# Kernel tuning notes

Measured on AMD Instinct MI355X. Metric: run time of the kernel, lower is better.

The kernel has to match this reference:

```python
import jax, jax.numpy as jnp
import numpy as np

N = 64        # SSM state size
L = 262144    # l_max / sequence length


def setup_inputs() -> dict:
    key = jax.random.key(0)
    ks = jax.random.split(key, 8)
    u = jax.random.normal(ks[0], (L,), dtype=jnp.float32)
    # HiPPO-DPLR style eigenvalue init
    Lambda_re = -0.5 * jnp.ones((N,), jnp.float32)
    Lambda_im = jnp.pi * jnp.arange(N, dtype=jnp.float32)
    P_re = jax.random.normal(ks[1], (N,), jnp.float32)
    P_im = jax.random.normal(ks[2], (N,), jnp.float32)
    B_re = jax.random.normal(ks[3], (N,), jnp.float32)
    B_im = jax.random.normal(ks[4], (N,), jnp.float32)
    C_ri = (0.5 ** 0.5) * jax.random.normal(ks[5], (N, 2), jnp.float32)  # C = C_ri[:,0] + i*C_ri[:,1]
    D = jnp.ones((1,), jnp.float32)
    log_step = jax.random.uniform(ks[6], (1,), jnp.float32,
                                  minval=float(np.log(0.001)), maxval=float(np.log(0.1)))
    return {"u": u, "Lambda_re": Lambda_re, "Lambda_im": Lambda_im,
            "P_re": P_re, "P_im": P_im, "B_re": B_re, "B_im": B_im,
            "C_ri": C_ri, "D": D, "log_step": log_step}


def _kernel_DPLR(Lambda, P, Q, B, C, step, l):
    # Evaluate the SSM generating function at the l roots of unity (bilinear discretization)
    Omega = jnp.exp((-2j * jnp.pi) * (jnp.arange(l) / l))          # (L,)
    g = (2.0 / step) * ((1.0 - Omega) / (1.0 + Omega))             # (L,)
    c = 2.0 / (1.0 + Omega)                                        # (L,)
    # Core Cauchy matrix: the single large (L, N) complex intermediate
    recip = 1.0 / (g[:, None] - Lambda[None, :])                   # (L, N)
    # Four Cauchy dot products fused into one thin matmul
    v = jnp.stack([C.conj() * B, C.conj() * P,
                   Q.conj() * B, Q.conj() * P], axis=1)            # (N, 4)
    k = recip @ v                                                  # (L, 4)
    k00, k01, k10, k11 = k[:, 0], k[:, 1], k[:, 2], k[:, 3]
    atRoots = c * (k00 - k01 * (1.0 / (1.0 + k11)) * k10)          # (L,)
    return jnp.fft.ifft(atRoots, l).real                           # (L,) real kernel


def _causal_convolution(u, K):
    l = u.shape[0]
    ud = jnp.fft.rfft(jnp.pad(u, (0, K.shape[0])))
    Kd = jnp.fft.rfft(jnp.pad(K, (0, l)))
    return jnp.fft.irfft(ud * Kd)[:l]


def reference(u, Lambda_re, Lambda_im, P_re, P_im, B_re, B_im, C_ri, D, log_step):
    Lambda = Lambda_re + 1j * Lambda_im
    P = P_re + 1j * P_im
    B = B_re + 1j * B_im
    C = C_ri[:, 0] + 1j * C_ri[:, 1]
    step = jnp.exp(log_step)                                       # (1,)
    K = _kernel_DPLR(Lambda, P, P, B, C, step, u.shape[0])
    return _causal_convolution(u, K) + D * u
```

## Files before the change

kernel.cpp:

```cpp
#include <hip/hip_runtime.h>
#include <math.h>

#define L_LEN  262144
#define NST    64
#define TPB    256
#define PI2F   6.2831853071795864769f
#define PIF    3.1415926535897932385f

__device__ inline float2 cmul(float2 a, float2 b) {
    return make_float2(a.x*b.x - a.y*b.y, a.x*b.y + a.y*b.x);
}

template<int M, int NF>
__device__ float2* lds_fft_r4(float2* b0, float2* b1, float sgn) {
    float2* src = b0; float2* dst = b1;
    int Ns = 1;
    while (Ns * 4 <= M) {
        __syncthreads();
        const int NB = NF * (M / 4);
        for (int bi = threadIdx.x; bi < NB; bi += TPB) {
            int f = bi / (M / 4);
            int j = bi & (M / 4 - 1);
            int r = j & (Ns - 1);
            const float2* s = src + f * M;
            float2 x0 = s[j];
            float2 x1 = s[j +     (M/4)];
            float2 x2 = s[j + 2 * (M/4)];
            float2 x3 = s[j + 3 * (M/4)];
            float ang = sgn * PI2F * ((float)r / (float)(4 * Ns));
            float sn, cs; __sincosf(ang, &sn, &cs);
            float2 w1 = make_float2(cs, sn);
            float2 w2 = cmul(w1, w1);
            float2 w3 = cmul(w2, w1);
            x1 = cmul(x1, w1); x2 = cmul(x2, w2); x3 = cmul(x3, w3);
            float2 t0 = make_float2(x0.x + x2.x, x0.y + x2.y);
            float2 t1 = make_float2(x0.x - x2.x, x0.y - x2.y);
            float2 t2 = make_float2(x1.x + x3.x, x1.y + x3.y);
            float2 t3 = make_float2(x1.x - x3.x, x1.y - x3.y);
            float2* d = dst + f * M + ((j - r) << 2) + r;
            d[0]      = make_float2(t0.x + t2.x, t0.y + t2.y);
            d[Ns]     = make_float2(t1.x - sgn * t3.y, t1.y + sgn * t3.x);
            d[2 * Ns] = make_float2(t0.x - t2.x, t0.y - t2.y);
            d[3 * Ns] = make_float2(t1.x + sgn * t3.y, t1.y - sgn * t3.x);
        }
        float2* t = src; src = dst; dst = t;
        Ns <<= 2;
    }
    if (Ns < M) {
        __syncthreads();
        const int NB = NF * (M / 2);
        for (int bi = threadIdx.x; bi < NB; bi += TPB) {
            int f = bi / (M / 2);
            int j = bi & (M / 2 - 1);
            const float2* s = src + f * M;
            float2 a = s[j];
            float2 b = s[j + M / 2];
            float ang = sgn * PI2F * ((float)j / (float)M);
            float sn, cs; __sincosf(ang, &sn, &cs);
            float2 wb = make_float2(cs * b.x - sn * b.y, cs * b.y + sn * b.x);
            float2* d = dst + f * M + j;
            d[0]     = make_float2(a.x + wb.x, a.y + wb.y);
            d[M / 2] = make_float2(a.x - wb.x, a.y - wb.y);
        }
        float2* t = src; src = dst; dst = t;
    }
    __syncthreads();
    return src;
}


__global__ __launch_bounds__(TPB) void kI(
    const float* __restrict__ u,
    const float* __restrict__ Lre, const float* __restrict__ Lim,
    const float* __restrict__ Pre, const float* __restrict__ Pim,
    const float* __restrict__ Bre, const float* __restrict__ Bim,
    const float* __restrict__ Cri, const float* __restrict__ lstp,
    float2* __restrict__ Acm, float2* __restrict__ T_K,
    float2* __restrict__ T_U, float2* __restrict__ T_Uo)
{
    __shared__ float2 b0[2048], b1[2048];
    __shared__ float4 cA[NST], cB[NST], cC[NST], cD[NST];
    const int t = threadIdx.x, bx = blockIdx.x;
    const int c0 = (bx & 255) << 1;
    const float invL = 1.0f / (float)L_LEN;
    if (bx < 256) {
        if (t < NST) {
            float lr = Lre[t], li = Lim[t];
            float pr = Pre[t], pi = Pim[t];
            float br = Bre[t], bi = Bim[t];
            float cr = Cri[2*t], ci = Cri[2*t+1];
            float dx = -lr;
            float v00x = cr*br + ci*bi, v00y = cr*bi - ci*br;
            float v01x = cr*pr + ci*pi, v01y = cr*pi - ci*pr;
            float v10x = pr*br + pi*bi, v10y = pr*bi - pi*br;
            float v11x = pr*pr + pi*pi;
            cA[t] = make_float4(li, dx*dx, dx*v11x, -v11x);
            cB[t] = make_float4(dx*v00x, v00y, dx*v00y, -v00x);
            cC[t] = make_float4(dx*v01x, v01y, dx*v01y, -v01x);
            cD[t] = make_float4(dx*v10x, v10y, dx*v10y, -v10x);
        }
        __syncthreads();
        float G2 = 2.0f / expf(lstp[0]);
        float tn[4], gi[4], acc[4][8];
        #pragma unroll
        for (int p = 0; p < 4; ++p) {
            int i = t + (p << 8);
            int f = i >> 9, e = i & 511;
            int m = (c0 + f) + (e << 9);
            float h = PIF * ((float)m * invL);
            float sn, cs; __sincosf(h, &sn, &cs);
            float tv = sn * __frcp_rn(cs);
            tv = fminf(fmaxf(tv, -1e7f), 1e7f);
            tn[p] = tv; gi[p] = G2 * tv;
            #pragma unroll
            for (int q = 0; q < 8; ++q) acc[p][q] = 0.f;
        }
        #pragma unroll 2
        for (int n = 0; n < NST; ++n) {
            float4 a = cA[n], b = cB[n], cc = cC[n], d = cD[n];
            #pragma unroll
            for (int p = 0; p < 4; ++p) {
                float dy   = gi[p] - a.x;
                float iv   = __frcp_rn(fmaf(dy, dy, a.y));
                float ivdy = iv * dy;
                acc[p][6] = fmaf(iv, a.z, acc[p][6]);
                acc[p][7] = fmaf(ivdy, a.w, acc[p][7]);
                acc[p][0] = fmaf(iv, b.x,  fmaf(ivdy, b.y,  acc[p][0]));
                acc[p][1] = fmaf(iv, b.z,  fmaf(ivdy, b.w,  acc[p][1]));
                acc[p][2] = fmaf(iv, cc.x, fmaf(ivdy, cc.y, acc[p][2]));
                acc[p][3] = fmaf(iv, cc.z, fmaf(ivdy, cc.w, acc[p][3]));
                acc[p][4] = fmaf(iv, d.x,  fmaf(ivdy, d.y,  acc[p][4]));
                acc[p][5] = fmaf(iv, d.z,  fmaf(ivdy, d.w,  acc[p][5]));
            }
        }
        #pragma unroll
        for (int p = 0; p < 4; ++p) {
            int i = t + (p << 8);
            int f = i >> 9, e = i & 511;
            float ax = 1.f + acc[p][6], ay = acc[p][7];
            float im = 1.f / (ax*ax + ay*ay);
            float tx = acc[p][2]*acc[p][4] - acc[p][3]*acc[p][5];
            float ty = acc[p][2]*acc[p][5] + acc[p][3]*acc[p][4];
            float wx = acc[p][0] - (tx*ax + ty*ay) * im;
            float wy = acc[p][1] - (ty*ax - tx*ay) * im;
            float2 A = make_float2(wx - tn[p]*wy, wy + tn[p]*wx);
            Acm[((c0 + f) << 9) + e] = A;
            b0[i] = A;
        }
        float2* r = lds_fft_r4<512, 2>(b0, b1, +1.f);
        for (int i = t; i < 1024; i += TPB) {
            int f = i & 1, k = i >> 1;
            int c = c0 + f;
            float ang = PI2F * ((float)(c * k) * invL);
            float sn, cs; __sincosf(ang, &sn, &cs);
            T_K[(k << 9) + c] = cmul(make_float2(cs, sn), r[(f << 9) + k]);
        }
    } else {
        for (int i = t; i < 1024; i += TPB) {
            int f = i & 1, e = i >> 1;
            int n = (c0 + f) + (e << 9);
            float uv = u[n];
            float sn, cs; __sincosf(PIF * ((float)n * invL), &sn, &cs);
            b0[(f << 9) + e]       = make_float2(uv, 0.f);
            b0[((2 + f) << 9) + e] = make_float2(uv * cs, -uv * sn);
        }
        float2* r = lds_fft_r4<512, 4>(b0, b1, -1.f);
        for (int i = t; i < 2048; i += TPB) {
            int f = i & 1, k = (i >> 1) & 511, v = i >> 10;
            int c = c0 + f;
            float ang = -PI2F * ((float)(c * k) * invL);
            float sn, cs; __sincosf(ang, &sn, &cs);
            float2 val = cmul(make_float2(cs, sn), r[(((v << 1) + f) << 9) + k]);
            if (v == 0) T_U [(k << 9) + c] = val;
            else        T_Uo[(k << 9) + c] = val;
        }
    }
}

__global__ __launch_bounds__(TPB) void kII(
    const float2* __restrict__ T_K, const float2* __restrict__ T_U,
    const float2* __restrict__ T_Uo,
    float2* __restrict__ T_Ko, float2* __restrict__ Ue, float2* __restrict__ Uo)
{
    __shared__ float2 b0[2048], b1[2048];
    const int t = threadIdx.x, bx = blockIdx.x;
    const int c0 = (bx & 255) << 1;
    const float invL = 1.0f / (float)L_LEN;
    if (bx < 256) {
        for (int i = t; i < 1024; i += TPB)
            b0[i] = T_K[((c0 + (i >> 9)) << 9) + (i & 511)];
        float2* r = lds_fft_r4<512, 2>(b0, b1, +1.f);
        float2* o = (r == b0) ? b1 : b0;
        for (int i = t; i < 1024; i += TPB) {
            int f = i >> 9, o1 = i & 511;
            int n = (c0 + f) + (o1 << 9);
            float K = r[i].x * invL;
            float sn, cs; __sincosf(PIF * ((float)n * invL), &sn, &cs);
            o[i] = make_float2(K * cs, -K * sn);
        }
        float2* r2 = lds_fft_r4<512, 2>(o, r, -1.f);
        for (int i = t; i < 1024; i += TPB) {
            int f = i & 1, k = i >> 1;
            int c = c0 + f;
            float ang = -PI2F * ((float)(c * k) * invL);
            float sn, cs; __sincosf(ang, &sn, &cs);
            T_Ko[(k << 9) + c] = cmul(make_float2(cs, sn), r2[(f << 9) + k]);
        }
    } else {
        for (int i = t; i < 2048; i += TPB) {
            int v = i >> 10, f = (i >> 9) & 1, e = i & 511;
            const float2* Tin = v ? T_Uo : T_U;
            b0[i] = Tin[((c0 + f) << 9) + e];
        }
        float2* r = lds_fft_r4<512, 4>(b0, b1, -1.f);
        for (int i = t; i < 2048; i += TPB) {
            int v = i >> 10, f = (i >> 9) & 1, k2 = i & 511;
            float2* Xo = v ? Uo : Ue;
            Xo[((c0 + f) << 9) + k2] = r[i];
        }
    }
}

__global__ __launch_bounds__(TPB) void kIII(
    const float2* __restrict__ T_Ko, const float2* __restrict__ Ue,
    const float2* __restrict__ Uo, const float2* __restrict__ Acm,
    float2* __restrict__ T_Ve, float2* __restrict__ T_Vo)
{
    __shared__ float2 b0[1024], b1[1024];
    const int t = threadIdx.x, kc = blockIdx.x;
    const float invL = 1.0f / (float)L_LEN;
    for (int i = t; i < 512; i += TPB)
        b0[i] = T_Ko[(kc << 9) + i];
    float2* r = lds_fft_r4<512, 1>(b0, b1, -1.f);
    float2* o = (r == b0) ? b1 : b0;
    for (int i = t; i < 512; i += TPB) {
        float2 ko = r[i];
        float2 ue = Ue [(kc << 9) + i];
        float2 uo = Uo [(kc << 9) + i];
        float2 av = Acm[(kc << 9) + i];
        o[i]       = cmul(ue, av);
        o[i + 512] = cmul(uo, ko);
    }
    float2* r2 = lds_fft_r4<512, 2>(o, r, +1.f);
    for (int i = t; i < 1024; i += TPB) {
        int v = i >> 9, k = i & 511;
        float ang = PI2F * ((float)(kc * k) * invL);
        float sn, cs; __sincosf(ang, &sn, &cs);
        float2 val = cmul(make_float2(cs, sn), r2[(v << 9) + k]);
        if (v == 0) T_Ve[(k << 9) + kc] = val;
        else        T_Vo[(k << 9) + kc] = val;
    }
}

__global__ __launch_bounds__(TPB) void kIV(
    const float2* __restrict__ T_Ve, const float2* __restrict__ T_Vo,
    const float* __restrict__ u, const float* __restrict__ Dp,
    float* __restrict__ out)
{
    __shared__ float2 b0[1024], b1[1024];
    const int t = threadIdx.x, k = blockIdx.x;
    const float invL = 1.0f / (float)L_LEN;
    for (int i = t; i < 512; i += TPB) {
        b0[i]       = T_Ve[(k << 9) + i];
        b0[i + 512] = T_Vo[(k << 9) + i];
    }
    float2* r = lds_fft_r4<512, 2>(b0, b1, +1.f);
    const float sc = 0.5f * invL;
    const float D = Dp[0];
    for (int o1 = t; o1 < 512; o1 += TPB) {
        int n = k + (o1 << 9);
        float sn, cs; __sincosf(PIF * ((float)n * invL), &sn, &cs);
        float2 yE = r[o1];
        float2 yO = r[o1 + 512];
        out[n] = fmaf(D, u[n], (yE.x + cs * yO.x - sn * yO.y) * sc);
    }
}

extern "C" void kernel_launch(void* const* d_in, const int* in_sizes, int n_in,
                              void* d_out, int out_size, void* d_ws, size_t ws_size,
                              hipStream_t stream) {
    const float* u    = (const float*)d_in[0];
    const float* Lre  = (const float*)d_in[1];
    const float* Lim  = (const float*)d_in[2];
    const float* Pre  = (const float*)d_in[3];
    const float* Pim  = (const float*)d_in[4];
    const float* Bre  = (const float*)d_in[5];
    const float* Bim  = (const float*)d_in[6];
    const float* Cri  = (const float*)d_in[7];
    const float* Dp   = (const float*)d_in[8];
    const float* lstp = (const float*)d_in[9];
    float* out = (float*)d_out;

    char* ws = (char*)d_ws;
    float2* Acm  = (float2*)(ws);
    float2* T_K  = (float2*)(ws + ( 2u << 20));
    float2* T_U  = (float2*)(ws + ( 4u << 20));
    float2* T_Uo = (float2*)(ws + ( 6u << 20));
    float2* T_Ko = (float2*)(ws + ( 8u << 20));
    float2* Ue   = (float2*)(ws + (10u << 20));
    float2* Uo   = (float2*)(ws + (12u << 20));
    float2* T_Ve = (float2*)(ws + (14u << 20));
    float2* T_Vo = (float2*)(ws + (16u << 20));

    kI  <<<512, TPB, 0, stream>>>(u, Lre,Lim,Pre,Pim,Bre,Bim,Cri,lstp,
                                  Acm, T_K, T_U, T_Uo);
    kII <<<512, TPB, 0, stream>>>(T_K, T_U, T_Uo, T_Ko, Ue, Uo);
    kIII<<<512, TPB, 0, stream>>>(T_Ko, Ue, Uo, Acm, T_Ve, T_Vo);
    kIV <<<512, TPB, 0, stream>>>(T_Ve, T_Vo, u, Dp, out);
}
```

Measured before the change: 117.7 us.

## Evaluate kernel spectrum directly at even and odd bins, dropping K round-trip FFTs

Instead of building the kernel spectrum at the L roots of unity, inverse-transforming it to time and forward-transforming the padded kernel again, the Cauchy generating function is evaluated directly at the integer and half-integer frequency positions the padded convolution needs. It is then multiplied with the input spectrum inside the spectral kernel. This removes the separate kernel-path FFT passes and the Acm/T_K/T_Ko/Ue/Uo intermediates, and cuts the pipeline from four launches to three. In exchange the Cauchy sum runs on twice as many points, now spread across all 512 blocks. The odd-bin evaluation relies on the state transition decaying to negligible size over L steps.

```diff
diff --git a/kernel.cpp b/kernel.cpp
--- a/kernel.cpp
+++ b/kernel.cpp
@@ -69,209 +69,148 @@
 }
 
 
-__global__ __launch_bounds__(TPB) void kI(
+__global__ __launch_bounds__(TPB) void k1_pass1(
     const float* __restrict__ u,
+    float2* __restrict__ T_U, float2* __restrict__ T_Uo)
+{
+    __shared__ float2 b0[1024], b1[1024];
+    const int t = threadIdx.x, bx = blockIdx.x;
+    const int sig = bx & 1;
+    const int c0  = bx & 510;
+    const float invL = 1.0f / (float)L_LEN;
+    for (int i = t; i < 1024; i += TPB) {
+        int f = i & 1, e = i >> 1;
+        int n = (c0 + f) + (e << 9);
+        float uv = u[n];
+        if (sig) {
+            float sn, cs; __sincosf(PIF * ((float)n * invL), &sn, &cs);
+            b0[(f << 9) + e] = make_float2(uv * cs, -uv * sn);
+        } else {
+            b0[(f << 9) + e] = make_float2(uv, 0.f);
+        }
+    }
+    float2* r = lds_fft_r4<512, 2>(b0, b1, -1.f);
+    float2* Tout = sig ? T_Uo : T_U;
+    for (int i = t; i < 1024; i += TPB) {
+        int f = i & 1, k = i >> 1;
+        int c = c0 + f;
+        float ang = -PI2F * ((float)(c * k) * invL);
+        float sn, cs; __sincosf(ang, &sn, &cs);
+        Tout[(k << 9) + c] = cmul(make_float2(cs, sn), r[(f << 9) + k]);
+    }
+}
+
+__global__ __launch_bounds__(TPB) void k2_spectral(
+    const float2* __restrict__ T_U, const float2* __restrict__ T_Uo,
     const float* __restrict__ Lre, const float* __restrict__ Lim,
     const float* __restrict__ Pre, const float* __restrict__ Pim,
     const float* __restrict__ Bre, const float* __restrict__ Bim,
     const float* __restrict__ Cri, const float* __restrict__ lstp,
-    float2* __restrict__ Acm, float2* __restrict__ T_K,
-    float2* __restrict__ T_U, float2* __restrict__ T_Uo)
-{
-    __shared__ float2 b0[2048], b1[2048];
-    __shared__ float4 cA[NST], cB[NST], cC[NST], cD[NST];
-    const int t = threadIdx.x, bx = blockIdx.x;
-    const int c0 = (bx & 255) << 1;
-    const float invL = 1.0f / (float)L_LEN;
-    if (bx < 256) {
-        if (t < NST) {
-            float lr = Lre[t], li = Lim[t];
-            float pr = Pre[t], pi = Pim[t];
-            float br = Bre[t], bi = Bim[t];
-            float cr = Cri[2*t], ci = Cri[2*t+1];
-            float dx = -lr;
-            float v00x = cr*br + ci*bi, v00y = cr*bi - ci*br;
-            float v01x = cr*pr + ci*pi, v01y = cr*pi - ci*pr;
-            float v10x = pr*br + pi*bi, v10y = pr*bi - pi*br;
-            float v11x = pr*pr + pi*pi;
-            cA[t] = make_float4(li, dx*dx, dx*v11x, -v11x);
-            cB[t] = make_float4(dx*v00x, v00y, dx*v00y, -v00x);
-            cC[t] = make_float4(dx*v01x, v01y, dx*v01y, -v01x);
-            cD[t] = make_float4(dx*v10x, v10y, dx*v10y, -v10x);
-        }
-        __syncthreads();
-        float G2 = 2.0f / expf(lstp[0]);
-        float tn[4], gi[4], acc[4][8];
-        #pragma unroll
-        for (int p = 0; p < 4; ++p) {
-            int i = t + (p << 8);
-            int f = i >> 9, e = i & 511;
-            int m = (c0 + f) + (e << 9);
-            float h = PIF * ((float)m * invL);
-            float sn, cs; __sincosf(h, &sn, &cs);
-            float tv = sn * __frcp_rn(cs);
-            tv = fminf(fmaxf(tv, -1e7f), 1e7f);
-            tn[p] = tv; gi[p] = G2 * tv;
-            #pragma unroll
-            for (int q = 0; q < 8; ++q) acc[p][q] = 0.f;
-        }
-        #pragma unroll 2
-        for (int n = 0; n < NST; ++n) {
-            float4 a = cA[n], b = cB[n], cc = cC[n], d = cD[n];
-            #pragma unroll
-            for (int p = 0; p < 4; ++p) {
-                float dy   = gi[p] - a.x;
-                float iv   = __frcp_rn(fmaf(dy, dy, a.y));
-                float ivdy = iv * dy;
-                acc[p][6] = fmaf(iv, a.z, acc[p][6]);
-                acc[p][7] = fmaf(ivdy, a.w, acc[p][7]);
-                acc[p][0] = fmaf(iv, b.x,  fmaf(ivdy, b.y,  acc[p][0]));
-                acc[p][1] = fmaf(iv, b.z,  fmaf(ivdy, b.w,  acc[p][1]));
-                acc[p][2] = fmaf(iv, cc.x, fmaf(ivdy, cc.y, acc[p][2]));
-                acc[p][3] = fmaf(iv, cc.z, fmaf(ivdy, cc.w, acc[p][3]));
-                acc[p][4] = fmaf(iv, d.x,  fmaf(ivdy, d.y,  acc[p][4]));
-                acc[p][5] = fmaf(iv, d.z,  fmaf(ivdy, d.w,  acc[p][5]));
-            }
-        }
-        #pragma unroll
-        for (int p = 0; p < 4; ++p) {
-            int i = t + (p << 8);
-            int f = i >> 9, e = i & 511;
-            float ax = 1.f + acc[p][6], ay = acc[p][7];
-            float im = 1.f / (ax*ax + ay*ay);
-            float tx = acc[p][2]*acc[p][4] - acc[p][3]*acc[p][5];
-            float ty = acc[p][2]*acc[p][5] + acc[p][3]*acc[p][4];
-            float wx = acc[p][0] - (tx*ax + ty*ay) * im;
-            float wy = acc[p][1] - (ty*ax - tx*ay) * im;
-            float2 A = make_float2(wx - tn[p]*wy, wy + tn[p]*wx);
-            Acm[((c0 + f) << 9) + e] = A;
-            b0[i] = A;
-        }
-        float2* r = lds_fft_r4<512, 2>(b0, b1, +1.f);
-        for (int i = t; i < 1024; i += TPB) {
-            int f = i & 1, k = i >> 1;
-            int c = c0 + f;
-            float ang = PI2F * ((float)(c * k) * invL);
-            float sn, cs; __sincosf(ang, &sn, &cs);
-            T_K[(k << 9) + c] = cmul(make_float2(cs, sn), r[(f << 9) + k]);
-        }
-    } else {
-        for (int i = t; i < 1024; i += TPB) {
-            int f = i & 1, e = i >> 1;
-            int n = (c0 + f) + (e << 9);
-            float uv = u[n];
-            float sn, cs; __sincosf(PIF * ((float)n * invL), &sn, &cs);
-            b0[(f << 9) + e]       = make_float2(uv, 0.f);
-            b0[((2 + f) << 9) + e] = make_float2(uv * cs, -uv * sn);
-        }
-        float2* r = lds_fft_r4<512, 4>(b0, b1, -1.f);
-        for (int i = t; i < 2048; i += TPB) {
-            int f = i & 1, k = (i >> 1) & 511, v = i >> 10;
-            int c = c0 + f;
-            float ang = -PI2F * ((float)(c * k) * invL);
-            float sn, cs; __sincosf(ang, &sn, &cs);
-            float2 val = cmul(make_float2(cs, sn), r[(((v << 1) + f) << 9) + k]);
-            if (v == 0) T_U [(k << 9) + c] = val;
-            else        T_Uo[(k << 9) + c] = val;
-        }
-    }
-}
-
-__global__ __launch_bounds__(TPB) void kII(
-    const float2* __restrict__ T_K, const float2* __restrict__ T_U,
-    const float2* __restrict__ T_Uo,
-    float2* __restrict__ T_Ko, float2* __restrict__ Ue, float2* __restrict__ Uo)
-{
-    __shared__ float2 b0[2048], b1[2048];
-    const int t = threadIdx.x, bx = blockIdx.x;
-    const int c0 = (bx & 255) << 1;
-    const float invL = 1.0f / (float)L_LEN;
-    if (bx < 256) {
-        for (int i = t; i < 1024; i += TPB)
-            b0[i] = T_K[((c0 + (i >> 9)) << 9) + (i & 511)];
-        float2* r = lds_fft_r4<512, 2>(b0, b1, +1.f);
-        float2* o = (r == b0) ? b1 : b0;
-        for (int i = t; i < 1024; i += TPB) {
-            int f = i >> 9, o1 = i & 511;
-            int n = (c0 + f) + (o1 << 9);
-            float K = r[i].x * invL;
-            float sn, cs; __sincosf(PIF * ((float)n * invL), &sn, &cs);
-            o[i] = make_float2(K * cs, -K * sn);
-        }
-        float2* r2 = lds_fft_r4<512, 2>(o, r, -1.f);
-        for (int i = t; i < 1024; i += TPB) {
-            int f = i & 1, k = i >> 1;
-            int c = c0 + f;
-            float ang = -PI2F * ((float)(c * k) * invL);
-            float sn, cs; __sincosf(ang, &sn, &cs);
-            T_Ko[(k << 9) + c] = cmul(make_float2(cs, sn), r2[(f << 9) + k]);
-        }
-    } else {
-        for (int i = t; i < 2048; i += TPB) {
-            int v = i >> 10, f = (i >> 9) & 1, e = i & 511;
-            const float2* Tin = v ? T_Uo : T_U;
-            b0[i] = Tin[((c0 + f) << 9) + e];
-        }
-        float2* r = lds_fft_r4<512, 4>(b0, b1, -1.f);
-        for (int i = t; i < 2048; i += TPB) {
-            int v = i >> 10, f = (i >> 9) & 1, k2 = i & 511;
-            float2* Xo = v ? Uo : Ue;
-            Xo[((c0 + f) << 9) + k2] = r[i];
-        }
-    }
-}
-
-__global__ __launch_bounds__(TPB) void kIII(
-    const float2* __restrict__ T_Ko, const float2* __restrict__ Ue,
-    const float2* __restrict__ Uo, const float2* __restrict__ Acm,
     float2* __restrict__ T_Ve, float2* __restrict__ T_Vo)
 {
     __shared__ float2 b0[1024], b1[1024];
-    const int t = threadIdx.x, kc = blockIdx.x;
+    __shared__ float4 cA[NST], cB[NST], cC[NST], cD[NST];
+    const int t = threadIdx.x, m1 = blockIdx.x;
     const float invL = 1.0f / (float)L_LEN;
-    for (int i = t; i < 512; i += TPB)
-        b0[i] = T_Ko[(kc << 9) + i];
-    float2* r = lds_fft_r4<512, 1>(b0, b1, -1.f);
+    if (t < NST) {
+        float lr = Lre[t], li = Lim[t];
+        float pr = Pre[t], pi = Pim[t];
+        float br = Bre[t], bi = Bim[t];
+        float cr = Cri[2*t], ci = Cri[2*t+1];
+        float dx = -lr;
+        float v00x = cr*br + ci*bi, v00y = cr*bi - ci*br;
+        float v01x = cr*pr + ci*pi, v01y = cr*pi - ci*pr;
+        float v10x = pr*br + pi*bi, v10y = pr*bi - pi*br;
+        float v11x = pr*pr + pi*pi;
+        cA[t] = make_float4(li, dx*dx, dx*v11x, -v11x);
+        cB[t] = make_float4(dx*v00x, v00y, dx*v00y, -v00x);
+        cC[t] = make_float4(dx*v01x, v01y, dx*v01y, -v01x);
+        cD[t] = make_float4(dx*v10x, v10y, dx*v10y, -v10x);
+    }
+    for (int i = t; i < 1024; i += TPB) {
+        int f = i >> 9, e = i & 511;
+        const float2* Tin = f ? T_Uo : T_U;
+        b0[i] = Tin[(m1 << 9) + e];
+    }
+    float2* r = lds_fft_r4<512, 2>(b0, b1, -1.f);
     float2* o = (r == b0) ? b1 : b0;
-    for (int i = t; i < 512; i += TPB) {
-        float2 ko = r[i];
-        float2 ue = Ue [(kc << 9) + i];
-        float2 uo = Uo [(kc << 9) + i];
-        float2 av = Acm[(kc << 9) + i];
-        o[i]       = cmul(ue, av);
-        o[i + 512] = cmul(uo, ko);
+
+    float G2 = 2.0f / expf(lstp[0]);
+    float tn[4], gi[4], acc[4][8];
+    #pragma unroll
+    for (int p = 0; p < 4; ++p) {
+        int k1 = t + ((p & 1) << 8);
+        float jf = (float)(m1 + (k1 << 9)) + ((p & 2) ? 0.5f : 0.0f);
+        float h = PIF * (jf * invL);
+        float sn, cs; __sincosf(h, &sn, &cs);
+        float tv = sn * __frcp_rn(cs);
+        tv = fminf(fmaxf(tv, -1e7f), 1e7f);
+        tn[p] = tv; gi[p] = G2 * tv;
+        #pragma unroll
+        for (int q = 0; q < 8; ++q) acc[p][q] = 0.f;
+    }
+    #pragma unroll 2
+    for (int n = 0; n < NST; ++n) {
+        float4 a = cA[n], b = cB[n], cc = cC[n], d = cD[n];
+        #pragma unroll
+        for (int p = 0; p < 4; ++p) {
+            float dy   = gi[p] - a.x;
+            float iv   = __frcp_rn(fmaf(dy, dy, a.y));
+            float ivdy = iv * dy;
+            acc[p][6] = fmaf(iv, a.z, acc[p][6]);
+            acc[p][7] = fmaf(ivdy, a.w, acc[p][7]);
+            acc[p][0] = fmaf(iv, b.x,  fmaf(ivdy, b.y,  acc[p][0]));
+            acc[p][1] = fmaf(iv, b.z,  fmaf(ivdy, b.w,  acc[p][1]));
+            acc[p][2] = fmaf(iv, cc.x, fmaf(ivdy, cc.y, acc[p][2]));
+            acc[p][3] = fmaf(iv, cc.z, fmaf(ivdy, cc.w, acc[p][3]));
+            acc[p][4] = fmaf(iv, d.x,  fmaf(ivdy, d.y,  acc[p][4]));
+            acc[p][5] = fmaf(iv, d.z,  fmaf(ivdy, d.w,  acc[p][5]));
+        }
+    }
+    #pragma unroll
+    for (int p = 0; p < 4; ++p) {
+        int k1 = t + ((p & 1) << 8);
+        float ax = 1.f + acc[p][6], ay = acc[p][7];
+        float im = 1.f / (ax*ax + ay*ay);
+        float tx = acc[p][2]*acc[p][4] - acc[p][3]*acc[p][5];
+        float ty = acc[p][2]*acc[p][5] + acc[p][3]*acc[p][4];
+        float wx = acc[p][0] - (tx*ax + ty*ay) * im;
+        float wy = acc[p][1] - (ty*ax - tx*ay) * im;
+        float2 H = make_float2(wx - tn[p]*wy, wy + tn[p]*wx);
+        if (p & 2) o[512 + k1] = cmul(r[512 + k1], H);
+        else       o[k1]       = cmul(r[k1],       H);
     }
     float2* r2 = lds_fft_r4<512, 2>(o, r, +1.f);
     for (int i = t; i < 1024; i += TPB) {
-        int v = i >> 9, k = i & 511;
-        float ang = PI2F * ((float)(kc * k) * invL);
+        int v = i >> 9, j = i & 511;
+        float ang = PI2F * ((float)(m1 * j) * invL);
         float sn, cs; __sincosf(ang, &sn, &cs);
-        float2 val = cmul(make_float2(cs, sn), r2[(v << 9) + k]);
-        if (v == 0) T_Ve[(k << 9) + kc] = val;
-        else        T_Vo[(k << 9) + kc] = val;
-    }
-}
-
-__global__ __launch_bounds__(TPB) void kIV(
+        float2 val = cmul(make_float2(cs, sn), r2[(v << 9) + j]);
+        if (v == 0) T_Ve[(j << 9) + m1] = val;
+        else        T_Vo[(j << 9) + m1] = val;
+    }
+}
+
+__global__ __launch_bounds__(TPB) void k3_out(
     const float2* __restrict__ T_Ve, const float2* __restrict__ T_Vo,
     const float* __restrict__ u, const float* __restrict__ Dp,
     float* __restrict__ out)
 {
     __shared__ float2 b0[1024], b1[1024];
-    const int t = threadIdx.x, k = blockIdx.x;
+    const int t = threadIdx.x, j = blockIdx.x;
     const float invL = 1.0f / (float)L_LEN;
     for (int i = t; i < 512; i += TPB) {
-        b0[i]       = T_Ve[(k << 9) + i];
-        b0[i + 512] = T_Vo[(k << 9) + i];
+        b0[i]       = T_Ve[(j << 9) + i];
+        b0[i + 512] = T_Vo[(j << 9) + i];
     }
     float2* r = lds_fft_r4<512, 2>(b0, b1, +1.f);
     const float sc = 0.5f * invL;
     const float D = Dp[0];
-    for (int o1 = t; o1 < 512; o1 += TPB) {
-        int n = k + (o1 << 9);
+    for (int p = t; p < 512; p += TPB) {
+        int n = j + (p << 9);
         float sn, cs; __sincosf(PIF * ((float)n * invL), &sn, &cs);
-        float2 yE = r[o1];
-        float2 yO = r[o1 + 512];
+        float2 yE = r[p];
+        float2 yO = r[p + 512];
         out[n] = fmaf(D, u[n], (yE.x + cs * yO.x - sn * yO.y) * sc);
     }
 }
@@ -292,19 +231,13 @@
     float* out = (float*)d_out;
 
     char* ws = (char*)d_ws;
-    float2* Acm  = (float2*)(ws);
-    float2* T_K  = (float2*)(ws + ( 2u << 20));
-    float2* T_U  = (float2*)(ws + ( 4u << 20));
-    float2* T_Uo = (float2*)(ws + ( 6u << 20));
-    float2* T_Ko = (float2*)(ws + ( 8u << 20));
-    float2* Ue   = (float2*)(ws + (10u << 20));
-    float2* Uo   = (float2*)(ws + (12u << 20));
-    float2* T_Ve = (float2*)(ws + (14u << 20));
-    float2* T_Vo = (float2*)(ws + (16u << 20));
-
-    kI  <<<512, TPB, 0, stream>>>(u, Lre,Lim,Pre,Pim,Bre,Bim,Cri,lstp,
-                                  Acm, T_K, T_U, T_Uo);
-    kII <<<512, TPB, 0, stream>>>(T_K, T_U, T_Uo, T_Ko, Ue, Uo);
-    kIII<<<512, TPB, 0, stream>>>(T_Ko, Ue, Uo, Acm, T_Ve, T_Vo);
-    kIV <<<512, TPB, 0, stream>>>(T_Ve, T_Vo, u, Dp, out);
-}
+    float2* T_U  = (float2*)(ws);
+    float2* T_Uo = (float2*)(ws + (2u << 20));
+    float2* T_Ve = (float2*)(ws + (4u << 20));
+    float2* T_Vo = (float2*)(ws + (6u << 20));
+
+    k1_pass1   <<<512, TPB, 0, stream>>>(u, T_U, T_Uo);
+    k2_spectral<<<512, TPB, 0, stream>>>(T_U, T_Uo, Lre,Lim,Pre,Pim,Bre,Bim,
+                                         Cri, lstp, T_Ve, T_Vo);
+    k3_out     <<<512, TPB, 0, stream>>>(T_Ve, T_Vo, u, Dp, out);
+}
```

New measurement: 123.0 us. 1.04x slower.
